# Optimization experiments

Hardware: AMD Instinct MI355X
Metric: run time of the kernel (lower is better)

Reference implementation:

```python
import jax, jax.numpy as jnp
import numpy as np

DIM_IN = 1024
DIM_OUT = 1024
NUM_HEADS = 16
HEAD_DIM = DIM_OUT // NUM_HEADS


def setup_inputs() -> dict:
    key = jax.random.key(0)
    ks = jax.random.split(key, 7)
    s = 1.0 / np.sqrt(DIM_IN)
    x = jax.random.normal(ks[0], (4, 2048, DIM_IN), dtype=jnp.float32)
    Wq = jax.random.uniform(ks[1], (DIM_IN, DIM_OUT), jnp.float32, -s, s)
    bq = jax.random.uniform(ks[2], (DIM_OUT,), jnp.float32, -s, s)
    Wk = jax.random.uniform(ks[3], (DIM_IN, DIM_OUT), jnp.float32, -s, s)
    bk = jax.random.uniform(ks[4], (DIM_OUT,), jnp.float32, -s, s)
    Wv = jax.random.uniform(ks[5], (DIM_IN, DIM_OUT), jnp.float32, -s, s)
    bv = jax.random.uniform(ks[6], (DIM_OUT,), jnp.float32, -s, s)
    return {"x": x, "Wq": Wq, "bq": bq, "Wk": Wk, "bk": bk, "Wv": Wv, "bv": bv}


def reference(x, Wq, bq, Wk, bk, Wv, bv):
    B, S, _ = x.shape
    scale = HEAD_DIM ** 0.5
    # project and split heads: [B, H, S, Dh]
    def heads(W, b):
        return (x @ W + b).reshape(B, S, NUM_HEADS, HEAD_DIM).transpose(0, 2, 1, 3)
    q = heads(Wq, bq)
    k = heads(Wk, bk)
    v = heads(Wv, bv)
    scores = jnp.einsum("bhqd,bhkd->bhqk", q, k) / scale  # [B,H,S,S]
    attn = jax.nn.softmax(scores, axis=-1)
    out = jnp.einsum("bhqk,bhkd->bhqd", attn, v)
    return out.transpose(0, 2, 1, 3).reshape(B, S, DIM_OUT)
```

## Files before the change

kernel.cpp:

```cpp
#include <hip/hip_runtime.h>
#include <hip/hip_bf16.h>


#define DIM  1024
#define SEQ  2048
#define BATCH 4
#define NH   16
#define HD   64

typedef __bf16 bf16x8 __attribute__((ext_vector_type(8)));
typedef short  s16x4  __attribute__((ext_vector_type(4)));
typedef float  f32x4  __attribute__((ext_vector_type(4)));
typedef unsigned int uint4v __attribute__((ext_vector_type(4)));

static __device__ __forceinline__ f32x4 mfma16(s16x4 a, s16x4 b, f32x4 c) {
    return __builtin_amdgcn_mfma_f32_16x16x16bf16_1k(a, b, c, 0, 0, 0);
}

static __device__ __forceinline__ unsigned short f2b(float f) {
    __bf16 h = (__bf16)f;
    return __builtin_bit_cast(unsigned short, h);
}

static __device__ __forceinline__ void load_lds16(const unsigned short* g,
                                                  unsigned short* l) {
    __builtin_amdgcn_global_load_lds(
        (const __attribute__((address_space(1))) void*)g,
        (__attribute__((address_space(3))) void*)l, 16, 0, 0);
}

__global__ __launch_bounds__(256) void cvt_x_k(const float* __restrict__ x,
                                               unsigned short* __restrict__ xb) {
    size_t i = ((size_t)blockIdx.x * 256 + threadIdx.x) * 8;
    const f32x4* s = (const f32x4*)(x + i);
    f32x4 a0 = s[0], a1 = s[1];
    bf16x8 v;
    for (int j = 0; j < 4; j++) { v[j] = (__bf16)a0[j]; v[4 + j] = (__bf16)a1[j]; }
    *(bf16x8*)(xb + i) = v;
}

__global__ void transpose_w_k(const float* __restrict__ Wq,
                              const float* __restrict__ Wk,
                              const float* __restrict__ Wv,
                              unsigned short* __restrict__ Wt) {
    __shared__ unsigned short t[32][33];
    int z = blockIdx.z;
    const float* W = (z == 0) ? Wq : (z == 1) ? Wk : Wv;
    unsigned short* o = Wt + (size_t)z * DIM * DIM;
    int tx = threadIdx.x;
    int n0 = blockIdx.x * 32, k0 = blockIdx.y * 32;
    for (int j = threadIdx.y; j < 32; j += 8)
        t[j][tx] = f2b(W[(size_t)(k0 + j) * DIM + n0 + tx]);
    __syncthreads();
    for (int j = threadIdx.y; j < 32; j += 8)
        o[(size_t)(n0 + j) * DIM + k0 + tx] = t[tx][j];
}

__global__ __launch_bounds__(512) void qkv_gemm_k(
    const unsigned short* __restrict__ xb,
    const unsigned short* __restrict__ WtBase,
    const float* __restrict__ bq,
    const float* __restrict__ bk,
    const float* __restrict__ bv,
    unsigned short* __restrict__ Qo,
    unsigned short* __restrict__ Ko,
    unsigned short* __restrict__ Vto) {
    __shared__ __align__(16) unsigned short As[256 * 64];
    __shared__ __align__(16) unsigned short Bs[128 * 64];
    int tid = threadIdx.x, wave = tid >> 6, lane = tid & 63;
    int quad = lane >> 4, lc = lane & 15;
    int bid = blockIdx.x;
    int xcd = bid & 7, slot = bid >> 3;
    int pp = slot / 24, i = slot - pp * 24;
    int p = pp * 8 + xcd;
    int z = i >> 3, nx = i & 7;
    int m0 = p * 256, n0 = nx * 128;
    const unsigned short* Wt = WtBase + (size_t)z * DIM * DIM;
    int wm = (wave >> 1) * 64, wn = (wave & 1) * 64;
    int swzlo = lc & 7;

    f32x4 acc[4][4] = {};

    for (int k0 = 0; k0 < DIM; k0 += 64) {
        __syncthreads();
        #pragma unroll
        for (int pI = 0; pI < 4; pI++) {
            int c = tid + pI * 512, r = c >> 3, cc = (c & 7) ^ (r & 7);
            load_lds16(xb + (size_t)(m0 + r) * DIM + k0 + cc * 8, &As[c * 8]);
        }
        #pragma unroll
        for (int pI = 0; pI < 2; pI++) {
            int c = tid + pI * 512, r = c >> 3, cc = (c & 7) ^ (r & 7);
            load_lds16(Wt + (size_t)(n0 + r) * DIM + k0 + cc * 8, &Bs[c * 8]);
        }
        __syncthreads();
        #pragma unroll
        for (int kk = 0; kk < 2; kk++) {
            int off = ((kk * 4 + quad) ^ swzlo) * 8;
            bf16x8 af[4], bfr[4];
            for (int mt = 0; mt < 4; mt++)
                af[mt] = *(const bf16x8*)&As[(wm + mt * 16 + lc) * 64 + off];
            for (int nt = 0; nt < 4; nt++)
                bfr[nt] = *(const bf16x8*)&Bs[(wn + nt * 16 + lc) * 64 + off];
            for (int mt = 0; mt < 4; mt++)
                for (int nt = 0; nt < 4; nt++)
                    acc[mt][nt] = __builtin_amdgcn_mfma_f32_16x16x32_bf16(
                        af[mt], bfr[nt], acc[mt][nt], 0, 0, 0);
        }
    }

    const float* bias = (z == 0) ? bq : (z == 1) ? bk : bv;
    float scale = (z == 0) ? 0.18033688011112042f : 1.0f;

    if (z != 2) {
        for (int nt = 0; nt < 4; nt++) {
            int n = n0 + wn + nt * 16 + lc;
            float bvl = bias[n];
            int h = n >> 6, d = n & 63;
            for (int mt = 0; mt < 4; mt++) {
                for (int r = 0; r < 4; r++) {
                    int m = m0 + wm + mt * 16 + quad * 4 + r;
                    int b = m >> 11, s = m & 2047;
                    unsigned short ub = f2b((acc[mt][nt][r] + bvl) * scale);
                    if (z == 0)
                        Qo[((size_t)(b * NH + h) * SEQ + s) * HD + d] = ub;
                    else
                        Ko[((size_t)(b * NH + h) * SEQ + s) * HD + d] = ub;
                }
            }
        }
    } else {
        __syncthreads();
        unsigned short* T = As + wave * 1024;
        int h = (n0 + wn) >> 6;
        int d = lane;
        for (int mt = 0; mt < 4; mt++) {
            for (int nt = 0; nt < 4; nt++) {
                int n = n0 + wn + nt * 16 + lc;
                float bvl = bias[n];
                s16x4 v4;
                for (int r = 0; r < 4; r++)
                    v4[r] = (short)f2b(acc[mt][nt][r] + bvl);
                *(s16x4*)&T[(nt * 16 + lc) * 16 + quad * 4] = v4;
            }
            int s_base = m0 + wm + mt * 16;
            int b = s_base >> 11, sl = s_base & 2047;
            unsigned short* dst =
                Vto + ((size_t)(b * NH + h) * HD + d) * SEQ + sl;
            uint4v t0 = *(const uint4v*)&T[d * 16];
            uint4v t1 = *(const uint4v*)&T[d * 16 + 8];
            *(uint4v*)&dst[0] = t0;
            *(uint4v*)&dst[8] = t1;
        }
    }
}

__global__ __launch_bounds__(512) void attn_k(
    const unsigned short* __restrict__ Q,
    const unsigned short* __restrict__ K,
    const unsigned short* __restrict__ Vt,
    float* __restrict__ out) {
    __shared__ __align__(16) unsigned short KV[2 * 8192];

    int tid = threadIdx.x, wave = tid >> 6, lane = tid & 63;
    int quad = lane >> 4, lc = lane & 15;
    int lc7 = lc & 7, lcb = lc >> 3;
    int bid = blockIdx.x;
    int j = bid >> 3;
    int bh = (bid & 7) * 8 + (j >> 3);
    int qt = j & 7;
    int b = bh >> 4, h = bh & 15;
    const unsigned short* Qg = Q + ((size_t)bh * SEQ + qt * 256) * HD;
    const unsigned short* Kg = K + (size_t)bh * SEQ * HD;
    const unsigned short* Vg = Vt + (size_t)bh * HD * SEQ;

    int sr = tid >> 3, scc = tid & 7;
    int kcc = scc ^ ((sr ^ (sr >> 3)) & 7);

    bf16x8 qf0[2], qf1[2];
    {
        const unsigned short* q0 = Qg + (size_t)(wave * 32 + lc) * HD + quad * 8;
        const unsigned short* q1 = q0 + 16 * HD;
        qf0[0] = *(const bf16x8*)q0;  qf0[1] = *(const bf16x8*)(q0 + 32);
        qf1[0] = *(const bf16x8*)q1;  qf1[1] = *(const bf16x8*)(q1 + 32);
    }

    f32x4 o[4][2] = {};
    f32x4 racc[2] = {};
    const s16x4 ones = {0x3F80, 0x3F80, 0x3F80, 0x3F80};

    {
        unsigned short* Ks = KV;
        unsigned short* Vs = KV + 4096;
        load_lds16(Kg + (size_t)sr * HD + kcc * 8, &Ks[tid * 8]);
        load_lds16(Vg + (size_t)sr * SEQ + kcc * 8, &Vs[tid * 8]);
    }

    for (int t0 = 0; t0 < SEQ; t0 += 64) {
        int cur = (t0 >> 6) & 1;
        unsigned short* Ks = KV + cur * 8192;
        unsigned short* Vs = Ks + 4096;
        __syncthreads();

        if (t0 + 64 < SEQ) {
            unsigned short* Kn = KV + (cur ^ 1) * 8192;
            unsigned short* Vn = Kn + 4096;
            load_lds16(Kg + (size_t)(t0 + 64 + sr) * HD + kcc * 8, &Kn[tid * 8]);
            load_lds16(Vg + (size_t)sr * SEQ + (t0 + 64) + kcc * 8, &Vn[tid * 8]);
        }

        s16x4 pf[4][2];
        __builtin_amdgcn_s_setprio(1);
        #pragma unroll
        for (int kt = 0; kt < 4; kt++) {
            int sk = lc7 ^ ((2 * kt + lcb) & 7);
            f32x4 sA = {}, sB = {};
            #pragma unroll
            for (int ks = 0; ks < 2; ks++) {
                bf16x8 kf = *(const bf16x8*)
                    &Ks[(kt * 16 + lc) * 64 + ((ks * 4 + quad) ^ sk) * 8];
                sA = __builtin_amdgcn_mfma_f32_16x16x32_bf16(kf, qf0[ks], sA, 0, 0, 0);
                sB = __builtin_amdgcn_mfma_f32_16x16x32_bf16(kf, qf1[ks], sB, 0, 0, 0);
            }
            #pragma unroll
            for (int r = 0; r < 4; r++) {
                float pa = __builtin_amdgcn_exp2f(sA[r]);
                float pb = __builtin_amdgcn_exp2f(sB[r]);
                pf[kt][0][r] = (short)f2b(pa);
                pf[kt][1][r] = (short)f2b(pb);
            }
            racc[0] = mfma16(ones, pf[kt][0], racc[0]);
            racc[1] = mfma16(ones, pf[kt][1], racc[1]);
        }

        #pragma unroll
        for (int dt = 0; dt < 4; dt++) {
            int sv = lc7 ^ ((2 * dt + lcb) & 7);
            #pragma unroll
            for (int kt = 0; kt < 4; kt++) {
                s16x4 vf = *(const s16x4*)
                    &Vs[(dt * 16 + lc) * 64 +
                        ((2 * kt + (quad >> 1)) ^ sv) * 8 + (quad & 1) * 4];
                o[dt][0] = mfma16(vf, pf[kt][0], o[dt][0]);
                o[dt][1] = mfma16(vf, pf[kt][1], o[dt][1]);
            }
        }
        __builtin_amdgcn_s_setprio(0);
    }

    float inv0 = 1.0f / racc[0][0];
    float inv1 = 1.0f / racc[1][0];

    float* o0 = out + ((size_t)b * SEQ + qt * 256 + wave * 32 + lc) * DIM
                + h * HD + quad * 4;
    float* o1 = o0 + (size_t)16 * DIM;
    #pragma unroll
    for (int dt = 0; dt < 4; dt++) {
        f32x4 s0 = o[dt][0]; s0 *= inv0;
        f32x4 s1 = o[dt][1]; s1 *= inv1;
        *(f32x4*)&o0[dt * 16] = s0;
        *(f32x4*)&o1[dt * 16] = s1;
    }
}

extern "C" void kernel_launch(void* const* d_in, const int* in_sizes, int n_in,
                              void* d_out, int out_size, void* d_ws, size_t ws_size,
                              hipStream_t stream) {
    (void)in_sizes; (void)n_in; (void)out_size; (void)ws_size;
    const float* x  = (const float*)d_in[0];
    const float* Wq = (const float*)d_in[1];
    const float* bq = (const float*)d_in[2];
    const float* Wk = (const float*)d_in[3];
    const float* bk = (const float*)d_in[4];
    const float* Wv = (const float*)d_in[5];
    const float* bv = (const float*)d_in[6];

    char* ws = (char*)d_ws;
    unsigned short* Wt = (unsigned short*)ws;
    unsigned short* Qb = (unsigned short*)(ws + (size_t)6 * 1024 * 1024);
    unsigned short* Kb = Qb + (size_t)BATCH * NH * SEQ * HD;
    unsigned short* Vb = Kb + (size_t)BATCH * NH * SEQ * HD;
    unsigned short* xb = (unsigned short*)d_out;

    cvt_x_k<<<dim3(4096), dim3(256), 0, stream>>>(x, xb);
    transpose_w_k<<<dim3(32, 32, 3), dim3(32, 8), 0, stream>>>(Wq, Wk, Wv, Wt);
    qkv_gemm_k<<<dim3(768), dim3(512), 0, stream>>>(xb, Wt, bq, bk, bv, Qb, Kb, Vb);
    attn_k<<<dim3(512), dim3(512), 0, stream>>>(Qb, Kb, Vb, (float*)d_out);
}
```

Baseline: 242.6 us.

## Switch attention inner loop to 32x32x16 bf16 MFMA with permlane32 swaps

Replaces the 16x16 MFMA tiling of QK^T, row-sum and PV with 32x32x16 bf16 MFMAs, so each wave handles a 32-query block with one f32x16 accumulator per 32 columns. The P fragments from the score MFMA are packed into bf16 pairs and rearranged across lane halves with v_permlane32_swap instead of being reused in 16x16 layout. This cuts the MFMA instruction count and LDS fragment reads per tile, at the cost of more cross-lane shuffling and a different swizzle and register layout.

```diff
diff --git a/kernel.cpp b/kernel.cpp
--- a/kernel.cpp
+++ b/kernel.cpp
@@ -11,10 +11,11 @@
 typedef __bf16 bf16x8 __attribute__((ext_vector_type(8)));
 typedef short  s16x4  __attribute__((ext_vector_type(4)));
 typedef float  f32x4  __attribute__((ext_vector_type(4)));
+typedef float  f32x16 __attribute__((ext_vector_type(16)));
 typedef unsigned int uint4v __attribute__((ext_vector_type(4)));
 
-static __device__ __forceinline__ f32x4 mfma16(s16x4 a, s16x4 b, f32x4 c) {
-    return __builtin_amdgcn_mfma_f32_16x16x16bf16_1k(a, b, c, 0, 0, 0);
+static __device__ __forceinline__ f32x16 mfma32(bf16x8 a, bf16x8 b, f32x16 c) {
+    return __builtin_amdgcn_mfma_f32_32x32x16_bf16(a, b, c, 0, 0, 0);
 }
 
 static __device__ __forceinline__ unsigned short f2b(float f) {
@@ -163,8 +164,7 @@
     __shared__ __align__(16) unsigned short KV[2 * 8192];
 
     int tid = threadIdx.x, wave = tid >> 6, lane = tid & 63;
-    int quad = lane >> 4, lc = lane & 15;
-    int lc7 = lc & 7, lcb = lc >> 3;
+    int l31 = lane & 31, hi = lane >> 5;
     int bid = blockIdx.x;
     int j = bid >> 3;
     int bh = (bid & 7) * 8 + (j >> 3);
@@ -177,17 +177,23 @@
     int sr = tid >> 3, scc = tid & 7;
     int kcc = scc ^ ((sr ^ (sr >> 3)) & 7);
 
-    bf16x8 qf0[2], qf1[2];
+    bf16x8 qf[4];
     {
-        const unsigned short* q0 = Qg + (size_t)(wave * 32 + lc) * HD + quad * 8;
-        const unsigned short* q1 = q0 + 16 * HD;
-        qf0[0] = *(const bf16x8*)q0;  qf0[1] = *(const bf16x8*)(q0 + 32);
-        qf1[0] = *(const bf16x8*)q1;  qf1[1] = *(const bf16x8*)(q1 + 32);
-    }
-
-    f32x4 o[4][2] = {};
-    f32x4 racc[2] = {};
-    const s16x4 ones = {0x3F80, 0x3F80, 0x3F80, 0x3F80};
+        const unsigned short* q0 = Qg + (size_t)(wave * 32 + l31) * HD + hi * 8;
+        #pragma unroll
+        for (int ds_ = 0; ds_ < 4; ds_++)
+            qf[ds_] = *(const bf16x8*)(q0 + ds_ * 16);
+    }
+
+    f32x16 o[2] = {};
+    f32x16 racc = {};
+    bf16x8 ones8;
+    #pragma unroll
+    for (int t = 0; t < 8; t++) ones8[t] = (__bf16)1.0f;
+
+    int swzK0 = ((l31 ^ (l31 >> 3)) & 7);
+    int r32 = 32 + l31;
+    int swzK1 = ((r32 ^ (r32 >> 3)) & 7);
 
     {
         unsigned short* Ks = KV;
@@ -209,57 +215,67 @@
             load_lds16(Vg + (size_t)sr * SEQ + (t0 + 64) + kcc * 8, &Vn[tid * 8]);
         }
 
-        s16x4 pf[4][2];
         __builtin_amdgcn_s_setprio(1);
         #pragma unroll
-        for (int kt = 0; kt < 4; kt++) {
-            int sk = lc7 ^ ((2 * kt + lcb) & 7);
-            f32x4 sA = {}, sB = {};
+        for (int kb = 0; kb < 2; kb++) {
+            int krow = kb * 32 + l31;
+            int ksw = (kb == 0) ? swzK0 : swzK1;
+            f32x16 sc = {};
             #pragma unroll
-            for (int ks = 0; ks < 2; ks++) {
-                bf16x8 kf = *(const bf16x8*)
-                    &Ks[(kt * 16 + lc) * 64 + ((ks * 4 + quad) ^ sk) * 8];
-                sA = __builtin_amdgcn_mfma_f32_16x16x32_bf16(kf, qf0[ks], sA, 0, 0, 0);
-                sB = __builtin_amdgcn_mfma_f32_16x16x32_bf16(kf, qf1[ks], sB, 0, 0, 0);
-            }
+            for (int ds_ = 0; ds_ < 4; ds_++) {
+                bf16x8 kfrag = *(const bf16x8*)
+                    &Ks[krow * 64 + ((ds_ * 2 + hi) ^ ksw) * 8];
+                sc = mfma32(kfrag, qf[ds_], sc);
+            }
+            unsigned int W[8];
             #pragma unroll
-            for (int r = 0; r < 4; r++) {
-                float pa = __builtin_amdgcn_exp2f(sA[r]);
-                float pb = __builtin_amdgcn_exp2f(sB[r]);
-                pf[kt][0][r] = (short)f2b(pa);
-                pf[kt][1][r] = (short)f2b(pb);
-            }
-            racc[0] = mfma16(ones, pf[kt][0], racc[0]);
-            racc[1] = mfma16(ones, pf[kt][1], racc[1]);
-        }
-
-        #pragma unroll
-        for (int dt = 0; dt < 4; dt++) {
-            int sv = lc7 ^ ((2 * dt + lcb) & 7);
+            for (int rr = 0; rr < 8; rr++) {
+                float p0 = __builtin_amdgcn_exp2f(sc[2 * rr]);
+                float p1 = __builtin_amdgcn_exp2f(sc[2 * rr + 1]);
+                W[rr] = ((unsigned)f2b(p1) << 16) | (unsigned)f2b(p0);
+            }
+            asm volatile("v_permlane32_swap_b32 %0, %1"
+                         : "+v"(W[0]), "+v"(W[2]));
+            asm volatile("v_permlane32_swap_b32 %0, %1"
+                         : "+v"(W[1]), "+v"(W[3]));
+            asm volatile("v_permlane32_swap_b32 %0, %1"
+                         : "+v"(W[4]), "+v"(W[6]));
+            asm volatile("v_permlane32_swap_b32 %0, %1"
+                         : "+v"(W[5]), "+v"(W[7]));
+            bf16x8 fA = __builtin_bit_cast(bf16x8,
+                            (uint4v){W[0], W[1], W[2], W[3]});
+            bf16x8 fB = __builtin_bit_cast(bf16x8,
+                            (uint4v){W[4], W[5], W[6], W[7]});
+            racc = mfma32(ones8, fA, racc);
+            racc = mfma32(ones8, fB, racc);
             #pragma unroll
-            for (int kt = 0; kt < 4; kt++) {
-                s16x4 vf = *(const s16x4*)
-                    &Vs[(dt * 16 + lc) * 64 +
-                        ((2 * kt + (quad >> 1)) ^ sv) * 8 + (quad & 1) * 4];
-                o[dt][0] = mfma16(vf, pf[kt][0], o[dt][0]);
-                o[dt][1] = mfma16(vf, pf[kt][1], o[dt][1]);
+            for (int db = 0; db < 2; db++) {
+                int vrow = db * 32 + l31;
+                int vsw = (db == 0) ? swzK0 : swzK1;
+                bf16x8 v0 = *(const bf16x8*)
+                    &Vs[vrow * 64 + ((kb * 4 + hi) ^ vsw) * 8];
+                bf16x8 v1 = *(const bf16x8*)
+                    &Vs[vrow * 64 + ((kb * 4 + 2 + hi) ^ vsw) * 8];
+                o[db] = mfma32(v0, fA, o[db]);
+                o[db] = mfma32(v1, fB, o[db]);
             }
         }
         __builtin_amdgcn_s_setprio(0);
     }
 
-    float inv0 = 1.0f / racc[0][0];
-    float inv1 = 1.0f / racc[1][0];
-
-    float* o0 = out + ((size_t)b * SEQ + qt * 256 + wave * 32 + lc) * DIM
-                + h * HD + quad * 4;
-    float* o1 = o0 + (size_t)16 * DIM;
+    float inv = 1.0f / racc[0];
+
+    float* orow = out + ((size_t)b * SEQ + qt * 256 + wave * 32 + l31) * DIM
+                  + h * HD + hi * 4;
     #pragma unroll
-    for (int dt = 0; dt < 4; dt++) {
-        f32x4 s0 = o[dt][0]; s0 *= inv0;
-        f32x4 s1 = o[dt][1]; s1 *= inv1;
-        *(f32x4*)&o0[dt * 16] = s0;
-        *(f32x4*)&o1[dt * 16] = s1;
+    for (int db = 0; db < 2; db++) {
+        #pragma unroll
+        for (int rr = 0; rr < 4; rr++) {
+            f32x4 s = { o[db][4 * rr], o[db][4 * rr + 1],
+                        o[db][4 * rr + 2], o[db][4 * rr + 3] };
+            s *= inv;
+            *(f32x4*)&orow[db * 32 + rr * 8] = s;
+        }
     }
 }
 
```

New measurement: 239.8 us. About the same (-1.2%).
